# Kernel tuning notes

Hardware: AMD Instinct MI355X
Metric: run time of the kernel (lower is better)

The kernel has to match this reference:

```python
import jax, jax.numpy as jnp
import numpy as np
from functools import partial

H = 128      # hidden size
IN = 86      # lstm input size (66 pose + 20 conditioning)
OUT = 66     # decoded pose dims
STEPS = 15   # rollout steps


def lstm_cell(u, h, c, Wih, Whh, b):
    # PyTorch gate order: i, f, g, o ; b = b_ih + b_hh precombined by caller
    gates = u @ Wih.T + h @ Whh.T + b          # [B, 4H]
    i, f, g, o = jnp.split(gates, 4, axis=-1)
    i = jax.nn.sigmoid(i)
    f = jax.nn.sigmoid(f)
    g = jnp.tanh(g)
    o = jax.nn.sigmoid(o)
    c = f * c + i * g
    h = o * jnp.tanh(c)
    return h, c


def setup_inputs() -> dict:
    key = jax.random.key(0)
    ks = jax.random.split(key, 12)
    B, T = 8192, 50
    k = 1.0 / np.sqrt(H)  # torch default uniform init bound
    u = lambda kk, shp: jax.random.uniform(kk, shp, jnp.float32, -k, k)
    return {
        "x": jax.random.normal(ks[0], (B, T, IN), jnp.float32),
        "Wih0": u(ks[1], (4 * H, IN)),
        "Whh0": u(ks[2], (4 * H, H)),
        "bih0": u(ks[3], (4 * H,)),
        "bhh0": u(ks[4], (4 * H,)),
        "Wih1": u(ks[5], (4 * H, H)),
        "Whh1": u(ks[6], (4 * H, H)),
        "bih1": u(ks[7], (4 * H,)),
        "bhh1": u(ks[8], (4 * H,)),
        "Wd": u(ks[9], (OUT, H)),
        "bd": u(ks[10], (OUT,)),
    }


def reference(x, Wih0, Whh0, bih0, bhh0, Wih1, Whh1, bih1, bhh1, Wd, bd):
    B = x.shape[0]
    b0 = bih0 + bhh0
    b1 = bih1 + bhh1

    def two_layer(state, u):
        h1, c1, h2, c2 = state
        h1, c1 = lstm_cell(u, h1, c1, Wih0, Whh0, b0)
        h2, c2 = lstm_cell(h1, h2, c2, Wih1, Whh1, b1)
        return (h1, c1, h2, c2), h2

    z = jnp.zeros((B, H), x.dtype)
    state0 = (z, z, z, z)

    # encode the history sequence; only final (h, c) matter
    state, _ = jax.lax.scan(lambda s, u: (two_layer(s, u)[0], None),
                            state0, jnp.swapaxes(x, 0, 1))

    cond = x[:, -1, OUT:]  # [B, 20] conditioning, held fixed during rollout

    # first rollout step uses the full last input frame
    state, h2 = two_layer(state, x[:, -1, :])
    pose0 = h2 @ Wd.T + bd  # [B, 66]

    def roll(carry, _):
        state, pose = carry
        u = jnp.concatenate([pose, cond], axis=-1)  # [B, 86]
        state, h2 = two_layer(state, u)
        pose = h2 @ Wd.T + bd
        return (state, pose), pose

    (_, _), rest = jax.lax.scan(roll, (state, pose0), None, length=STEPS - 1)
    # rest: [14, B, 66] -> stack with pose0 along time
    out = jnp.concatenate([pose0[:, None, :], jnp.swapaxes(rest, 0, 1)], axis=1)
    return out  # [B, 15, 66]
```

## Files before the change

### kernel.cpp

```cpp
#include <hip/hip_runtime.h>
#include <cstdint>
#include <cstddef>

#define H_    128
#define IN_   86
#define OUT_  66
#define T_    50
#define B_    8192
#define NPOSE 15

#define K0T 7
#define K1T 8
#define KDT 4
#define NTD 5
#define S0  232
#define S1  264
#define BR  32
#define THR 512
#define RING 12

#define B0P_OFF 0
#define B0P_SZ  (K0T * 32 * 1024)
#define B1P_OFF (B0P_OFF + B0P_SZ)
#define B1P_SZ  (K1T * 32 * 1024)
#define BDP_OFF (B1P_OFF + B1P_SZ)
#define BDP_SZ  (KDT * NTD * 1024)
#define B0P_N (B0P_SZ / 2)
#define B1P_N (B1P_SZ / 2)
#define TOT_N ((B0P_SZ + B1P_SZ + BDP_SZ) / 2)

typedef __attribute__((ext_vector_type(8))) _Float16 hfrag;
typedef __attribute__((ext_vector_type(4))) float   ffrag;

#define MFMA16(AC, AA, BB) \
  AC = __builtin_amdgcn_mfma_f32_16x16x32_f16((AA), (BB), (AC), 0, 0, 0)

template <int N> struct IC { static constexpr int value = N; };
template <int N, class F>
__device__ __forceinline__ void cfor(F&& f) {
  if constexpr (N > 0) {
    cfor<N - 1>(static_cast<F&&>(f));
    f(IC<N - 1>{});
  }
}

template<int MODE>
constexpr int kt_of() { return MODE==0?15: MODE==1?12: MODE==2?8: MODE==3?3: 7; }

template <int N>
__device__ __forceinline__ void waitvm() {
  asm volatile("s_waitcnt vmcnt(%0)" :: "i"(N) : "memory");
}

__device__ __forceinline__ void gload_lds16(const void* g, void* l) {
  __builtin_amdgcn_global_load_lds(
      (const __attribute__((address_space(1))) unsigned int*)g,
      (__attribute__((address_space(3))) unsigned int*)l,
      16, 0, 0);
}

__device__ __forceinline__ unsigned short f16rn(float f) {
  union { _Float16 h; unsigned short u; } cv;
  cv.h = (_Float16)f;
  return cv.u;
}
__device__ __forceinline__ float sigmoid_f(float v) {
  return __fdividef(1.f, 1.f + __expf(-v));
}
__device__ __forceinline__ float tanh_f(float v) {
  float av = fabsf(v);
  float e  = __expf(-2.f * av);
  float t  = __fdividef(1.f - e, 1.f + e);
  return copysignf(t, v);
}

__global__ void wm_prep(
    const float* __restrict__ Wih0, const float* __restrict__ Whh0,
    const float* __restrict__ Wih1, const float* __restrict__ Whh1,
    const float* __restrict__ Wd,
    unsigned short* __restrict__ wsu)
{
  const int idx = blockIdx.x * 256 + threadIdx.x;
  if (idx >= TOT_N) return;
  int region, l;
  if (idx < B0P_N)               { region = 0; l = idx; }
  else if (idx < B0P_N + B1P_N)  { region = 1; l = idx - B0P_N; }
  else                           { region = 2; l = idx - (B0P_N + B1P_N); }

  int k, nt, lane, j;
  if (region < 2) {
    k  = l >> 14;
    int r1 = l & 16383;
    nt = r1 >> 9;
    int li = r1 & 511;
    lane = li >> 3; j = li & 7;
  } else {
    k  = l / 2560;
    int r1 = l % 2560;
    nt = r1 >> 9;
    int li = r1 & 511;
    lane = li >> 3; j = li & 7;
  }
  const int n  = nt * 16 + (lane & 15);
  const int kk = k * 32 + (lane >> 4) * 8 + j;

  float v = 0.f;
  if (region == 0) {
    if (kk < IN_)                    v = Wih0[n * IN_ + kk];
    else if (kk >= 96 && kk < 224)   v = Whh0[n * H_ + (kk - 96)];
  } else if (region == 1) {
    v = (kk < H_) ? Wih1[n * H_ + kk] : Whh1[n * H_ + (kk - H_)];
  } else {
    if (n < OUT_)                    v = Wd[n * H_ + kk];
  }
  wsu[idx] = f16rn(v);
}

__global__ __launch_bounds__(THR, 2) void wm_main(
    const float* __restrict__ x,
    const char*  __restrict__ wsb,
    const float* __restrict__ bih0, const float* __restrict__ bhh0,
    const float* __restrict__ bih1, const float* __restrict__ bhh1,
    const float* __restrict__ bd,
    float* __restrict__ out)
{
  __shared__ __align__(16) unsigned short A0h[BR * S0];
  __shared__ __align__(16) unsigned short A1h[BR * S1];
  __shared__ __align__(16) char RG[8][RING * 1024];

  const int tid  = threadIdx.x;
  const int lane = tid & 63;
  const int uw   = tid >> 6;
  const int ln15 = lane & 15;
  const int quad = lane >> 4;
  const int quad4 = quad * 4;
  const int lane16 = lane * 16;

  const char* B0 = wsb + B0P_OFF;
  const char* B1 = wsb + B1P_OFF;
  const char* BD = wsb + BDP_OFF;
  char* myring = &RG[uw][0];
  const _Float16* A0f = (const _Float16*)A0h;
  const _Float16* A1f = (const _Float16*)A1h;

  for (int i = tid; i < BR * S0; i += THR) A0h[i] = 0;
  for (int i = tid; i < BR * S1; i += THR) A1h[i] = 0;

  float b0r[4], b1r[4];
  #pragma unroll
  for (int g = 0; g < 4; ++g) {
    const int n = g * 128 + uw * 16 + ln15;
    b0r[g] = bih0[n] + bhh0[n];
    b1r[g] = bih1[n] + bhh1[n];
  }
  const int od = uw * 16 + ln15;
  const float bdr = (uw < NTD && od < OUT_) ? bd[od] : 0.f;

  float c1[2][4], c2[2][4];
  #pragma unroll
  for (int m = 0; m < 2; ++m)
    #pragma unroll
    for (int r = 0; r < 4; ++r) { c1[m][r] = 0.f; c2[m][r] = 0.f; }

  const int a0b0 = ln15 * S0 + quad * 8;
  const int a0b1 = (16 + ln15) * S0 + quad * 8;
  const int a1b0 = ln15 * S1 + quad * 8;
  const int a1b1 = (16 + ln15) * S1 + quad * 8;
  const int unit = uw * 16 + ln15;
  const int xr_row = tid >> 4;
  const int xr_col = tid & 15;

  ffrag acc0[2][4], acc1[2][4];

  auto binit0 = [&]() {
    #pragma unroll
    for (int m = 0; m < 2; ++m)
      #pragma unroll
      for (int g = 0; g < 4; ++g) acc0[m][g] = (ffrag){b0r[g], b0r[g], b0r[g], b0r[g]};
  };
  auto binit1 = [&]() {
    #pragma unroll
    for (int m = 0; m < 2; ++m)
      #pragma unroll
      for (int g = 0; g < 4; ++g) acc1[m][g] = (ffrag){b1r[g], b1r[g], b1r[g], b1r[g]};
  };
  auto pw_l1 = [&]() {
    #pragma unroll
    for (int m = 0; m < 2; ++m)
      #pragma unroll
      for (int rr = 0; rr < 4; ++rr) {
        const float ig = sigmoid_f(acc0[m][0][rr]);
        const float fg = sigmoid_f(acc0[m][1][rr]);
        const float gg = tanh_f(acc0[m][2][rr]);
        const float og = sigmoid_f(acc0[m][3][rr]);
        const float c  = fmaf(fg, c1[m][rr], ig * gg);
        c1[m][rr] = c;
        const float h  = og * tanh_f(c);
        const unsigned short hv = f16rn(h);
        const int row = m * 16 + quad4 + rr;
        A0h[row * S0 + 96 + unit] = hv;
        A1h[row * S1 + unit]      = hv;
      }
  };
  auto pw_l2 = [&]() {
    #pragma unroll
    for (int m = 0; m < 2; ++m)
      #pragma unroll
      for (int rr = 0; rr < 4; ++rr) {
        const float ig = sigmoid_f(acc1[m][0][rr]);
        const float fg = sigmoid_f(acc1[m][1][rr]);
        const float gg = tanh_f(acc1[m][2][rr]);
        const float og = sigmoid_f(acc1[m][3][rr]);
        const float c  = fmaf(fg, c2[m][rr], ig * gg);
        c2[m][rr] = c;
        const float h  = og * tanh_f(c);
        const int row = m * 16 + quad4 + rr;
        A1h[row * S1 + 128 + unit] = f16rn(h);
      }
  };

  auto issue_jt = [&](auto mc2, auto jc2) {
    constexpr int MODE = decltype(mc2)::value;
    constexpr int i = decltype(jc2)::value;
    constexpr bool i1 = (MODE <= 2) && (i < K1T);
    constexpr int ik = MODE==0 ? (i1 ? i : i - 8)
                     : MODE==1 ? (i1 ? i : 3 + (i - 8))
                     : i;
    constexpr int ISB = (4 * i) % RING;
    const char* src = (i1 ? B1 : B0) + (size_t)ik * 32 * 1024;
    #pragma unroll
    for (int g = 0; g < 4; ++g)
      gload_lds16(src + (size_t)(g * 8 + uw) * 1024 + lane16,
                  myring + (ISB + g) * 1024);
  };
  auto prefetch_g = [&](auto mc2) {
    constexpr int MODE = decltype(mc2)::value;
    constexpr int NP = kt_of<MODE>() < 3 ? kt_of<MODE>() : 3;
    cfor<NP>([&](auto jc) { issue_jt(mc2, jc); });
  };

  auto run_gemm = [&](auto mc, auto pfc) {
    constexpr int MODE = decltype(mc)::value;
    constexpr bool PF = decltype(pfc)::value != 0;
    constexpr int KT = kt_of<MODE>();
    if constexpr (!PF) prefetch_g(mc);
    cfor<KT>([&](auto jc) {
      constexpr int j = decltype(jc)::value;
      constexpr bool is1 = (MODE <= 2) && (j < K1T);
      constexpr int k = MODE==0 ? (is1 ? j : j - 8)
                      : MODE==1 ? (is1 ? j : 3 + (j - 8))
                      : j;
      constexpr int REM = KT - 1 - j;
      constexpr int W = 4 * (REM < 2 ? REM : 2);
      waitvm<W>();
      hfrag a0, a1;
      if constexpr (is1) {
        a0 = *(const hfrag*)(A1f + a1b0 + k * 32);
        a1 = *(const hfrag*)(A1f + a1b1 + k * 32);
      } else {
        a0 = *(const hfrag*)(A0f + a0b0 + k * 32);
        a1 = *(const hfrag*)(A0f + a0b1 + k * 32);
      }
      constexpr int SB = (4 * j) % RING;
      __builtin_amdgcn_s_setprio(1);
      #pragma unroll
      for (int g = 0; g < 4; ++g) {
        const hfrag bh = *(const hfrag*)(myring + (SB + g) * 1024 + lane16);
        if constexpr (is1) { MFMA16(acc1[0][g], a0, bh); MFMA16(acc1[1][g], a1, bh); }
        else               { MFMA16(acc0[0][g], a0, bh); MFMA16(acc0[1][g], a1, bh); }
      }
      __builtin_amdgcn_s_setprio(0);
      if constexpr (j + 3 < KT) issue_jt(mc, IC<j + 3>{});
    });
  };

  auto barrier2 = [&]() {
    asm volatile("s_waitcnt lgkmcnt(0)" ::: "memory");
    __builtin_amdgcn_s_barrier();
    asm volatile("" ::: "memory");
  };

  auto stage_x = [&](int t) {
    const float* xr = x + ((size_t)(blockIdx.x * BR + xr_row) * T_ + t) * IN_;
    float xv[6];
    #pragma unroll
    for (int m = 0; m < 6; ++m) {
      const int k = xr_col + m * 16;
      xv[m] = (k < IN_) ? xr[k] : 0.f;
    }
    #pragma unroll
    for (int m = 0; m < 6; ++m) {
      const int k = xr_col + m * 16;
      if (k < IN_) A0h[xr_row * S0 + k] = f16rn(xv[m]);
    }
  };

  barrier2();

  stage_x(0);
  prefetch_g(IC<4>{});
  barrier2();
  binit0();
  run_gemm(IC<4>{}, IC<1>{});
  barrier2();

  for (int t = 0; t < T_; ++t) {
    prefetch_g(IC<0>{});
    if (t < T_ - 1) {
      stage_x(t + 1);
      if (t > 0) pw_l2();
      pw_l1();
    } else {
      if (t > 0) pw_l2();
      pw_l1();
    }
    barrier2();

    binit1();
    binit0();
    run_gemm(IC<0>{}, IC<1>{});
    barrier2();
  }

  for (int t = T_; t < T_ + NPOSE; ++t) {
    const bool more = (t < T_ + NPOSE - 1);
    prefetch_g(IC<2>{});
    if (t == T_) pw_l2();
    pw_l1();
    barrier2();

    binit1();
    if (more) { binit0(); run_gemm(IC<1>{}, IC<1>{}); }
    else      { run_gemm(IC<2>{}, IC<1>{}); }
    barrier2();

    pw_l2();
    barrier2();

    const int s = t - T_;
    if (uw < NTD) {
      ffrag d0 = (ffrag){bdr, bdr, bdr, bdr};
      ffrag d1 = (ffrag){bdr, bdr, bdr, bdr};
      #pragma unroll
      for (int k = 0; k < KDT; ++k) {
        const hfrag ah0 = *(const hfrag*)(A1f + a1b0 + 128 + k * 32);
        const hfrag ah1 = *(const hfrag*)(A1f + a1b1 + 128 + k * 32);
        const hfrag bh  = *(const hfrag*)(BD + (size_t)(k * NTD + uw) * 1024 + lane16);
        MFMA16(d0, ah0, bh);
        MFMA16(d1, ah1, bh);
      }
      if (od < OUT_) {
        #pragma unroll
        for (int m = 0; m < 2; ++m)
          #pragma unroll
          for (int rr = 0; rr < 4; ++rr) {
            const int row = m * 16 + quad4 + rr;
            const float v = m ? d1[rr] : d0[rr];
            out[((size_t)(blockIdx.x * BR + row) * NPOSE + s) * OUT_ + od] = v;
            if (s < NPOSE - 1) A0h[row * S0 + od] = f16rn(v);
          }
      }
    }
    barrier2();

    if (more) run_gemm(IC<3>{}, IC<0>{});
  }
}

extern "C" void kernel_launch(void* const* d_in, const int* in_sizes, int n_in,
                              void* d_out, int out_size, void* d_ws, size_t ws_size,
                              hipStream_t stream)
{
  const float* x    = (const float*)d_in[0];
  const float* Wih0 = (const float*)d_in[1];
  const float* Whh0 = (const float*)d_in[2];
  const float* bih0 = (const float*)d_in[3];
  const float* bhh0 = (const float*)d_in[4];
  const float* Wih1 = (const float*)d_in[5];
  const float* Whh1 = (const float*)d_in[6];
  const float* bih1 = (const float*)d_in[7];
  const float* bhh1 = (const float*)d_in[8];
  const float* Wd   = (const float*)d_in[9];
  const float* bd   = (const float*)d_in[10];

  wm_prep<<<(TOT_N + 255) / 256, 256, 0, stream>>>(Wih0, Whh0, Wih1, Whh1, Wd,
                                                   (unsigned short*)d_ws);
  wm_main<<<B_ / BR, THR, 0, stream>>>(x, (const char*)d_ws,
                                       bih0, bhh0, bih1, bhh1, bd,
                                       (float*)d_out);
}
```

Before: 1.340 ms.

## Deepen weight prefetch ring and overlap x and decoder loads with pointwise work

The LDS ring for weight tiles grows from 12 to 16 slots, so the GEMM keeps four k-tiles in flight instead of three. Loads of the next x frame are issued before the pointwise LSTM work and written to LDS after it, and decoder weight fragments are loaded into registers early. The mode-3 GEMM prefetch is moved ahead of pw_l2 in the rollout. Loads of x and stores of the output use nontemporal hints. The aim is to hide global-load latency in the sequential recurrence, at the cost of more LDS and registers, which may lower occupancy.

Result: slower. 1.368 ms (+2.1%).

```diff
diff --git a/kernel.cpp b/kernel.cpp
--- a/kernel.cpp
+++ b/kernel.cpp
@@ -17,7 +17,7 @@
 #define S1  264
 #define BR  32
 #define THR 512
-#define RING 12
+#define RING 16
 
 #define B0P_OFF 0
 #define B0P_SZ  (K0T * 32 * 1024)
@@ -235,7 +235,7 @@
   };
   auto prefetch_g = [&](auto mc2) {
     constexpr int MODE = decltype(mc2)::value;
-    constexpr int NP = kt_of<MODE>() < 3 ? kt_of<MODE>() : 3;
+    constexpr int NP = kt_of<MODE>() < 4 ? kt_of<MODE>() : 4;
     cfor<NP>([&](auto jc) { issue_jt(mc2, jc); });
   };
 
@@ -251,7 +251,7 @@
                       : MODE==1 ? (is1 ? j : 3 + (j - 8))
                       : j;
       constexpr int REM = KT - 1 - j;
-      constexpr int W = 4 * (REM < 2 ? REM : 2);
+      constexpr int W = 4 * (REM < 3 ? REM : 3);
       waitvm<W>();
       hfrag a0, a1;
       if constexpr (is1) {
@@ -270,7 +270,7 @@
         else               { MFMA16(acc0[0][g], a0, bh); MFMA16(acc0[1][g], a1, bh); }
       }
       __builtin_amdgcn_s_setprio(0);
-      if constexpr (j + 3 < KT) issue_jt(mc, IC<j + 3>{});
+      if constexpr (j + 4 < KT) issue_jt(mc, IC<j + 4>{});
     });
   };
 
@@ -280,24 +280,22 @@
     asm volatile("" ::: "memory");
   };
 
-  auto stage_x = [&](int t) {
-    const float* xr = x + ((size_t)(blockIdx.x * BR + xr_row) * T_ + t) * IN_;
+  barrier2();
+
+  {
+    const float* xr = x + ((size_t)(blockIdx.x * BR + xr_row) * T_ + 0) * IN_;
     float xv[6];
     #pragma unroll
     for (int m = 0; m < 6; ++m) {
       const int k = xr_col + m * 16;
-      xv[m] = (k < IN_) ? xr[k] : 0.f;
+      xv[m] = (k < IN_) ? __builtin_nontemporal_load(xr + k) : 0.f;
     }
     #pragma unroll
     for (int m = 0; m < 6; ++m) {
       const int k = xr_col + m * 16;
       if (k < IN_) A0h[xr_row * S0 + k] = f16rn(xv[m]);
     }
-  };
-
-  barrier2();
-
-  stage_x(0);
+  }
   prefetch_g(IC<4>{});
   barrier2();
   binit0();
@@ -305,14 +303,26 @@
   barrier2();
 
   for (int t = 0; t < T_; ++t) {
+    float xv[6];
+    const bool stg = (t < T_ - 1);
+    if (stg) {
+      const float* xr = x + ((size_t)(blockIdx.x * BR + xr_row) * T_ + (t + 1)) * IN_;
+      #pragma unroll
+      for (int m = 0; m < 6; ++m) {
+        const int k = xr_col + m * 16;
+        xv[m] = (k < IN_) ? __builtin_nontemporal_load(xr + k) : 0.f;
+      }
+      __builtin_amdgcn_sched_barrier(0);
+    }
     prefetch_g(IC<0>{});
-    if (t < T_ - 1) {
-      stage_x(t + 1);
-      if (t > 0) pw_l2();
-      pw_l1();
-    } else {
-      if (t > 0) pw_l2();
-      pw_l1();
+    if (t > 0) pw_l2();
+    pw_l1();
+    if (stg) {
+      #pragma unroll
+      for (int m = 0; m < 6; ++m) {
+        const int k = xr_col + m * 16;
+        if (k < IN_) A0h[xr_row * S0 + k] = f16rn(xv[m]);
+      }
     }
     barrier2();
 
@@ -334,6 +344,14 @@
     else      { run_gemm(IC<2>{}, IC<1>{}); }
     barrier2();
 
+    hfrag bdreg[4];
+    if (uw < NTD) {
+      #pragma unroll
+      for (int k = 0; k < KDT; ++k)
+        bdreg[k] = *(const hfrag*)(BD + (size_t)(k * NTD + uw) * 1024 + lane16);
+    }
+    __builtin_amdgcn_sched_barrier(0);
+    if (more) prefetch_g(IC<3>{});
     pw_l2();
     barrier2();
 
@@ -345,9 +363,8 @@
       for (int k = 0; k < KDT; ++k) {
         const hfrag ah0 = *(const hfrag*)(A1f + a1b0 + 128 + k * 32);
         const hfrag ah1 = *(const hfrag*)(A1f + a1b1 + 128 + k * 32);
-        const hfrag bh  = *(const hfrag*)(BD + (size_t)(k * NTD + uw) * 1024 + lane16);
-        MFMA16(d0, ah0, bh);
-        MFMA16(d1, ah1, bh);
+        MFMA16(d0, ah0, bdreg[k]);
+        MFMA16(d1, ah1, bdreg[k]);
       }
       if (od < OUT_) {
         #pragma unroll
@@ -356,14 +373,15 @@
           for (int rr = 0; rr < 4; ++rr) {
             const int row = m * 16 + quad4 + rr;
             const float v = m ? d1[rr] : d0[rr];
-            out[((size_t)(blockIdx.x * BR + row) * NPOSE + s) * OUT_ + od] = v;
+            __builtin_nontemporal_store(
+                v, out + ((size_t)(blockIdx.x * BR + row) * NPOSE + s) * OUT_ + od);
             if (s < NPOSE - 1) A0h[row * S0 + od] = f16rn(v);
           }
       }
     }
     barrier2();
 
-    if (more) run_gemm(IC<3>{}, IC<0>{});
+    if (more) run_gemm(IC<3>{}, IC<1>{});
   }
 }
 
```
